# Kernel tuning notes

Hardware: AMD Instinct MI355X
Metric: run time of the kernel (lower is better)

Reference implementation:

```python
import jax, jax.numpy as jnp
import numpy as np

N_NODES = 50000
N_EDGES = 800000
IN_CH, HID_CH, OUT_CH = 128, 128, 64


def _gcn_conv(x, W, b, src, dst, n):
    """PyG GCNConv: self-loops + symmetric norm + linear + scatter-add + bias."""
    loop = jnp.arange(n, dtype=src.dtype)
    src_sl = jnp.concatenate([src, loop])  # [E+N]
    dst_sl = jnp.concatenate([dst, loop])
    # degree computed on edges incl. self-loops (edge weight 1)
    deg = jax.ops.segment_sum(jnp.ones_like(dst_sl, dtype=x.dtype), dst_sl,
                              num_segments=n)
    dinv = jnp.where(deg > 0, jax.lax.rsqrt(deg), 0.0)
    norm = dinv[src_sl] * dinv[dst_sl]  # [E+N]
    xw = x @ W  # [N, F_out]
    msg = xw[src_sl] * norm[:, None]  # gather + scale, [E+N, F_out]
    out = jax.ops.segment_sum(msg, dst_sl, num_segments=n)
    return out + b


def setup_inputs() -> dict:
    key = jax.random.key(0)
    ks = jax.random.split(key, 5)
    x = jax.random.normal(ks[0], (N_NODES, IN_CH), dtype=jnp.float32)
    edge_index = jax.random.randint(ks[1], (2, N_EDGES), 0, N_NODES, dtype=jnp.int64)
    s1 = 1.0 / np.sqrt(IN_CH)
    s2 = 1.0 / np.sqrt(HID_CH)
    W1 = jax.random.normal(ks[2], (IN_CH, HID_CH), dtype=jnp.float32) * s1
    W2 = jax.random.normal(ks[3], (HID_CH, HID_CH), dtype=jnp.float32) * s2
    W3 = jax.random.normal(ks[4], (HID_CH, OUT_CH), dtype=jnp.float32) * s2
    return {
        "x": x, "edge_index": edge_index,
        "W1": W1, "b1": jnp.zeros((HID_CH,), jnp.float32),
        "W2": W2, "b2": jnp.zeros((HID_CH,), jnp.float32),
        "W3": W3, "b3": jnp.zeros((OUT_CH,), jnp.float32),
    }


def reference(x, edge_index, W1, b1, W2, b2, W3, b3):
    n = x.shape[0]
    src, dst = edge_index[0], edge_index[1]
    # dropout(p=0.6) is identity in eval mode
    h = jax.nn.relu(_gcn_conv(x, W1, b1, src, dst, n))
    h = jax.nn.relu(_gcn_conv(h, W2, b2, src, dst, n))
    out = _gcn_conv(h, W3, b3, src, dst, n)
    return out
```

## Files before the change

kernel.cpp:

```cpp
#include <hip/hip_runtime.h>
#include <cstdint>

#define IN_CH 128
#define HID_CH 128
#define OUT_CH 64
#define NB 49
#define CAP 32768
#define CHUNK 2048

typedef __attribute__((ext_vector_type(8))) short bf8_t;
typedef __attribute__((ext_vector_type(4))) float f4_t;

__device__ __forceinline__ uint32_t f_to_bf(float f) {
    union { float f; uint32_t u; } v; v.f = f;
    uint32_t u = v.u;
    return (u + 0x7fffu + ((u >> 16) & 1u)) >> 16;
}
__device__ __forceinline__ float bf_to_f(uint32_t h) {
    union { uint32_t u; float f; } v; v.u = h << 16; return v.f;
}
__device__ __forceinline__ float2 bf2_to_f2(uint32_t u) {
    union { uint32_t u; float f; } a, b;
    a.u = u << 16; b.u = u & 0xffff0000u;
    float2 r; r.x = a.f; r.y = b.f; return r;
}

__device__ __forceinline__ int detect64(const int* __restrict__ e32) {
    return (e32[1] | e32[3] | e32[5] | e32[7]) == 0;
}
__device__ __forceinline__ int edge_at(const void* edges, int is64, int idx) {
    if (is64) return (int)((const long long*)edges)[idx];
    return ((const int*)edges)[idx];
}

__global__ void init_cursors_kernel(int* __restrict__ bucket_cur) {
    int t = threadIdx.x;
    if (t < 64) bucket_cur[t] = t * CAP;
}

__global__ __launch_bounds__(256) void scatter_kernel(
    const void* __restrict__ ei, int* __restrict__ bucket_cur,
    int2* __restrict__ buckets, int E) {
    __shared__ int cnt[64];
    int tid = threadIdx.x;
    int base = blockIdx.x * CHUNK;
    int is64 = detect64((const int*)ei);
    if (tid < 64) cnt[tid] = 0;
    __syncthreads();
    int dloc[8];
#pragma unroll
    for (int it = 0; it < 8; it++) {
        int i = base + it * 256 + tid;
        int d = (i < E) ? edge_at(ei, is64, E + i) : -1;
        dloc[it] = d;
        if (d >= 0) atomicAdd(&cnt[d >> 10], 1);
    }
    __syncthreads();
    if (tid < 64) {
        int v = cnt[tid];
        cnt[tid] = atomicAdd(&bucket_cur[tid], v);
    }
    __syncthreads();
#pragma unroll
    for (int it = 0; it < 8; it++) {
        int i = base + it * 256 + tid;
        if (dloc[it] >= 0) {
            int s = edge_at(ei, is64, i);
            int p = atomicAdd(&cnt[dloc[it] >> 10], 1);
            buckets[p] = make_int2(s, dloc[it]);
        }
    }
}

__global__ __launch_bounds__(512) void csr_local_kernel(
    const int2* __restrict__ buckets, const int* __restrict__ bucket_cur,
    int* __restrict__ row_ptr, int* __restrict__ bsum, float* __restrict__ dinv, int n) {
    __shared__ int cnt[1024];
    __shared__ int sb[1024];
    int b = blockIdx.x, tid = threadIdx.x;
    int base = b << 10;
    int lim = min(1024, n - base);
    if (lim <= 0) { if (tid == 0) bsum[b] = 0; return; }
    int ecnt = bucket_cur[b] - b * CAP;
    const int2* ebase = buckets + (size_t)b * CAP;
    for (int i = tid; i < 1024; i += 512) cnt[i] = 0;
    __syncthreads();
    for (int i = tid; i < ecnt; i += 512)
        atomicAdd(&cnt[ebase[i].y - base], 1);
    __syncthreads();
    for (int i = tid; i < lim; i += 512)
        dinv[base + i] = rsqrtf((float)(cnt[i] + 1));
    __syncthreads();
    int* a = cnt; int* s = sb;
    for (int st = 1; st < 1024; st <<= 1) {
        for (int i = tid; i < 1024; i += 512)
            s[i] = a[i] + ((i >= st) ? a[i - st] : 0);
        __syncthreads();
        int* t = a; a = s; s = t;
    }
    for (int i = tid; i < lim; i += 512)
        row_ptr[base + i] = (i > 0) ? a[i - 1] : 0;
    if (tid == 0) bsum[b] = a[1023];
}

__global__ void scan_totals_kernel(const int* __restrict__ bsum, int* __restrict__ boff,
                                   int* __restrict__ row_ptr, int nb, int n) {
    int lane = threadIdx.x;
    int v = (lane < nb) ? bsum[lane] : 0;
    int incl = v;
#pragma unroll
    for (int off = 1; off < 64; off <<= 1) {
        int t = __shfl_up(incl, off);
        if (lane >= off) incl += t;
    }
    if (lane < nb) boff[lane] = incl - v;
    if (lane == 63) row_ptr[n] = incl;
}

__global__ __launch_bounds__(512) void fill_bucket_kernel(
    const int2* __restrict__ buckets, const int* __restrict__ bucket_cur,
    int* __restrict__ row_ptr, const int* __restrict__ boff,
    int* __restrict__ col, int n) {
    __shared__ int cur[1024];
    int b = blockIdx.x, tid = threadIdx.x;
    int base = b << 10;
    int lim = min(1024, n - base);
    if (lim <= 0) return;
    int ecnt = bucket_cur[b] - b * CAP;
    const int2* ebase = buckets + (size_t)b * CAP;
    int bo = boff[b];
    for (int i = tid; i < lim; i += 512) {
        int v = row_ptr[base + i] + bo;
        row_ptr[base + i] = v;
        cur[i] = v;
    }
    __syncthreads();
    for (int i = tid; i < ecnt; i += 512) {
        int2 e = ebase[i];
        int p = atomicAdd(&cur[e.y - base], 1);
        col[p] = e.x;
    }
}

__global__ void w_split_all(const float* __restrict__ W1, const float* __restrict__ W2,
                            const float* __restrict__ W3,
                            uint16_t* w1h, uint16_t* w1l, uint16_t* w2h, uint16_t* w2l,
                            uint16_t* w3h, uint16_t* w3l) {
    int idx = blockIdx.x * blockDim.x + threadIdx.x;
    const float* W; uint16_t* oh; uint16_t* ol; int FOUT; int e;
    if (idx < 16384)      { W = W1; oh = w1h; ol = w1l; FOUT = 128; e = idx; }
    else if (idx < 32768) { W = W2; oh = w2h; ol = w2l; FOUT = 128; e = idx - 16384; }
    else if (idx < 40960) { W = W3; oh = w3h; ol = w3l; FOUT = 64;  e = idx - 32768; }
    else return;
    int j = e & 7;
    int lane = (e >> 3) & 63;
    int rem = e >> 9;
    int NT = FOUT >> 4;
    int nt = rem % NT, kc = rem / NT;
    int k = kc * 32 + ((lane >> 4) << 3) + j;
    int c = nt * 16 + (lane & 15);
    float v = W[(size_t)k * FOUT + c];
    uint32_t h = f_to_bf(v);
    uint32_t l = f_to_bf(v - bf_to_f(h));
    oh[e] = (uint16_t)h;
    ol[e] = (uint16_t)l;
}

template <int FOUT, bool BFOUT, bool AF32>
__global__ __launch_bounds__(256) void gemm_mfma(
    const void* __restrict__ A0, const uint16_t* __restrict__ Alo,
    const uint16_t* __restrict__ Wfhi, const uint16_t* __restrict__ Wflo,
    const float* __restrict__ dinv, void* __restrict__ Yv, int n) {
    constexpr int NT = FOUT / 16;
    constexpr int NTW = 2;
    int wid = threadIdx.x >> 6;
    int lane = threadIdx.x & 63;
    int cp, tile0, tstride;
    if (FOUT == 128) { cp = wid;     tile0 = blockIdx.x;                  tstride = gridDim.x; }
    else             { cp = wid & 1; tile0 = blockIdx.x * 2 + (wid >> 1); tstride = gridDim.x * 2; }
    int ntiles = (n + 15) >> 4;

    bf8_t wh[NTW][4], wl[NTW][4];
#pragma unroll
    for (int t = 0; t < NTW; t++) {
        int nt = cp * NTW + t;
#pragma unroll
        for (int kc = 0; kc < 4; kc++) {
            size_t b = ((size_t)(kc * NT + nt) * 64 + lane) * 8;
            wh[t][kc] = *(const bf8_t*)&Wfhi[b];
            wl[t][kc] = *(const bf8_t*)&Wflo[b];
        }
    }
    int row_in = lane & 15;
    int koff = (lane >> 4) << 3;
    int colb = lane & 15;
    int rq = (lane >> 4) << 2;

    for (int tile = tile0; tile < ntiles; tile += tstride) {
        int R = tile << 4;
        int arow = R + row_in; if (arow >= n) arow = n - 1;
        bf8_t ah[4], al[4];
        if (AF32) {
            const float* ap = (const float*)A0 + (size_t)arow * 128 + koff;
#pragma unroll
            for (int kc = 0; kc < 4; kc++) {
                float4 pv = *(const float4*)(ap + kc * 32);
                float4 qv = *(const float4*)(ap + kc * 32 + 4);
                float vv[8] = {pv.x, pv.y, pv.z, pv.w, qv.x, qv.y, qv.z, qv.w};
#pragma unroll
                for (int j = 0; j < 8; j++) {
                    uint32_t h = f_to_bf(vv[j]);
                    ah[kc][j] = (short)h;
                    al[kc][j] = (short)f_to_bf(vv[j] - bf_to_f(h));
                }
            }
        } else {
            const uint16_t* ap_hi = (const uint16_t*)A0 + (size_t)arow * 128 + koff;
            const uint16_t* ap_lo = Alo + (size_t)arow * 128 + koff;
#pragma unroll
            for (int kc = 0; kc < 4; kc++) {
                ah[kc] = *(const bf8_t*)(ap_hi + kc * 32);
                al[kc] = *(const bf8_t*)(ap_lo + kc * 32);
            }
        }
        f4_t acc[NTW];
#pragma unroll
        for (int t = 0; t < NTW; t++) acc[t] = (f4_t){0.f, 0.f, 0.f, 0.f};
#pragma unroll
        for (int kc = 0; kc < 4; kc++) {
#pragma unroll
            for (int t = 0; t < NTW; t++) {
                acc[t] = __builtin_amdgcn_mfma_f32_16x16x32_bf16(ah[kc], wh[t][kc], acc[t], 0, 0, 0);
                acc[t] = __builtin_amdgcn_mfma_f32_16x16x32_bf16(ah[kc], wl[t][kc], acc[t], 0, 0, 0);
                acc[t] = __builtin_amdgcn_mfma_f32_16x16x32_bf16(al[kc], wh[t][kc], acc[t], 0, 0, 0);
            }
        }
#pragma unroll
        for (int t = 0; t < NTW; t++) {
            int c = (cp * NTW + t) * 16 + colb;
#pragma unroll
            for (int r = 0; r < 4; r++) {
                int row = R + rq + r;
                if (row < n) {
                    float v = acc[t][r] * dinv[row];
                    if (BFOUT)
                        ((uint16_t*)Yv)[(size_t)row * FOUT + c] = (uint16_t)f_to_bf(v);
                    else
                        ((float*)Yv)[(size_t)row * FOUT + c] = v;
                }
            }
        }
    }
}

template <int CH, bool RELU, int OUTMODE>
__global__ __launch_bounds__(256) void aggregate_kernel(
    const void* __restrict__ Yv, const int* __restrict__ row_ptr,
    const int* __restrict__ col, const float* __restrict__ dinv,
    const float* __restrict__ bias, void* __restrict__ out0,
    void* __restrict__ out1, int n) {
    int w = blockIdx.x * 4 + (threadIdx.x >> 6);
    int lane = threadIdx.x & 63;
    if (w >= n) return;
    constexpr int V = CH / 64;

    auto loadrow = [&](int node) -> float2 {
        if (V == 2) {
            uint32_t u = *((const uint32_t*)Yv + (size_t)node * (CH / 2) + lane);
            return bf2_to_f2(u);
        } else {
            uint32_t u = ((const uint16_t*)Yv)[(size_t)node * CH + lane];
            float2 r; r.x = bf_to_f(u); r.y = 0.f;
            return r;
        }
    };

    float2 acc[8];
#pragma unroll
    for (int t = 0; t < 8; t++) acc[t] = (float2){0.f, 0.f};
    acc[0] = loadrow(w);
    int start = row_ptr[w], end = row_ptr[w + 1];
    for (int base = start; base < end; base += 64) {
        int cnt = min(64, end - base);
        int sv = (base + lane < end) ? col[base + lane] : 0;
        int j = 0;
        for (; j + 8 <= cnt; j += 8) {
            int s[8];
#pragma unroll
            for (int t = 0; t < 8; t++) s[t] = __shfl(sv, j + t);
            float2 v[8];
#pragma unroll
            for (int t = 0; t < 8; t++) v[t] = loadrow(s[t]);
#pragma unroll
            for (int t = 0; t < 8; t++) { acc[t].x += v[t].x; acc[t].y += v[t].y; }
        }
        for (; j + 2 <= cnt; j += 2) {
            int s0 = __shfl(sv, j), s1 = __shfl(sv, j + 1);
            float2 v0 = loadrow(s0), v1 = loadrow(s1);
            acc[0].x += v0.x; acc[0].y += v0.y;
            acc[1].x += v1.x; acc[1].y += v1.y;
        }
        for (; j < cnt; j++) {
            int s = __shfl(sv, j);
            float2 v = loadrow(s);
            acc[0].x += v.x; acc[0].y += v.y;
        }
    }
    float sx = ((acc[0].x + acc[1].x) + (acc[2].x + acc[3].x)) +
               ((acc[4].x + acc[5].x) + (acc[6].x + acc[7].x));
    float sy = ((acc[0].y + acc[1].y) + (acc[2].y + acc[3].y)) +
               ((acc[4].y + acc[5].y) + (acc[6].y + acc[7].y));
    float di = dinv[w];
    if (V == 2) {
        float ox = sx * di + bias[lane * 2];
        float oy = sy * di + bias[lane * 2 + 1];
        if (RELU) { ox = fmaxf(ox, 0.f); oy = fmaxf(oy, 0.f); }
        if (OUTMODE == 0) {
            float2 o; o.x = ox; o.y = oy;
            *(float2*)((float*)out0 + (size_t)w * CH + lane * 2) = o;
        } else {
            uint32_t h0 = f_to_bf(ox), h1 = f_to_bf(oy);
            uint32_t l0 = f_to_bf(ox - bf_to_f(h0)), l1 = f_to_bf(oy - bf_to_f(h1));
            ((uint32_t*)out0)[(size_t)w * (CH / 2) + lane] = h0 | (h1 << 16);
            ((uint32_t*)out1)[(size_t)w * (CH / 2) + lane] = l0 | (l1 << 16);
        }
    } else {
        float ox = sx * di + bias[lane];
        if (RELU) ox = fmaxf(ox, 0.f);
        ((float*)out0)[(size_t)w * CH + lane] = ox;
    }
}

extern "C" void kernel_launch(void* const* d_in, const int* in_sizes, int n_in,
                              void* d_out, int out_size, void* d_ws, size_t ws_size,
                              hipStream_t stream) {
    const float* x  = (const float*)d_in[0];
    const void*  ei = d_in[1];
    const float* W1 = (const float*)d_in[2];
    const float* b1 = (const float*)d_in[3];
    const float* W2 = (const float*)d_in[4];
    const float* b2 = (const float*)d_in[5];
    const float* W3 = (const float*)d_in[6];
    const float* b3 = (const float*)d_in[7];
    int n = in_sizes[0] / IN_CH;
    int E = in_sizes[1] / 2;

    char* p = (char*)d_ws;
    auto carve = [&](size_t bytes) {
        char* r = p;
        p += (bytes + 255) & ~(size_t)255;
        return r;
    };
    float*    dinv       = (float*)carve((size_t)n * 4);
    int*      row_ptr    = (int*)carve((size_t)(n + 1) * 4);
    int*      bsum       = (int*)carve(64 * 4);
    int*      boff       = (int*)carve(64 * 4);
    int*      bucket_cur = (int*)carve(64 * 4);
    int*      col        = (int*)carve((size_t)E * 4);
    char*     bucket_mem = carve((size_t)NB * CAP * 8);
    int2*     buckets    = (int2*)bucket_mem;
    void*     y          = (void*)bucket_mem;
    uint16_t* ahi        = (uint16_t*)carve((size_t)n * 128 * 2);
    uint16_t* alo        = (uint16_t*)carve((size_t)n * 128 * 2);
    uint16_t* w1h        = (uint16_t*)carve(128 * 128 * 2);
    uint16_t* w1l        = (uint16_t*)carve(128 * 128 * 2);
    uint16_t* w2h        = (uint16_t*)carve(128 * 128 * 2);
    uint16_t* w2l        = (uint16_t*)carve(128 * 128 * 2);
    uint16_t* w3h        = (uint16_t*)carve(128 * 64 * 2);
    uint16_t* w3l        = (uint16_t*)carve(128 * 64 * 2);

    const int tpb = 256;
    int sb = (E + CHUNK - 1) / CHUNK;

    init_cursors_kernel<<<1, 64, 0, stream>>>(bucket_cur);
    scatter_kernel<<<sb, tpb, 0, stream>>>(ei, bucket_cur, buckets, E);
    csr_local_kernel<<<NB, 512, 0, stream>>>(buckets, bucket_cur, row_ptr, bsum, dinv, n);
    scan_totals_kernel<<<1, 64, 0, stream>>>(bsum, boff, row_ptr, NB, n);
    fill_bucket_kernel<<<NB, 512, 0, stream>>>(buckets, bucket_cur, row_ptr, boff, col, n);
    w_split_all<<<160, tpb, 0, stream>>>(W1, W2, W3, w1h, w1l, w2h, w2l, w3h, w3l);

    int gb = 782;
    int ab = (n + 3) / 4;

    gemm_mfma<128, true, true><<<gb, 256, 0, stream>>>(x, nullptr, w1h, w1l, dinv, y, n);
    aggregate_kernel<128, true, 1><<<ab, 256, 0, stream>>>(y, row_ptr, col, dinv, b1, ahi, alo, n);
    gemm_mfma<128, true, false><<<gb, 256, 0, stream>>>(ahi, alo, w2h, w2l, dinv, y, n);
    aggregate_kernel<128, true, 1><<<ab, 256, 0, stream>>>(y, row_ptr, col, dinv, b2, ahi, alo, n);
    gemm_mfma<64, true, false><<<gb, 256, 0, stream>>>(ahi, alo, w3h, w3l, dinv, y, n);
    aggregate_kernel<64, false, 0><<<ab, 256, 0, stream>>>(y, row_ptr, col, dinv, b3, d_out, nullptr, n);
}
```

Before: 283.2 us.

## Fuse aggregation with next-layer GEMM and overlap edge scatter with first GEMM

Merges the init-cursor kernel into the weight-split kernel. Runs the edge bucket scatter and the first-layer GEMM in one launch, with the GEMM no longer scaling by dinv because dinv is not yet known at that point. Each aggregate kernel now stages its 16 aggregated rows (hi/lo bf16) in shared memory and immediately runs the next layer's MFMA GEMM. This removes the round trip of the hidden activations through global memory and cuts the launch count. The cost is per-edge dinv[src] loads in the first aggregation and fewer neighbour accumulators.

```diff
diff --git a/kernel.cpp b/kernel.cpp
--- a/kernel.cpp
+++ b/kernel.cpp
@@ -1,10 +1,6 @@
 #include <hip/hip_runtime.h>
 #include <cstdint>
 
-#define IN_CH 128
-#define HID_CH 128
-#define OUT_CH 64
-#define NB 49
 #define CAP 32768
 #define CHUNK 2048
 
@@ -33,42 +29,136 @@
     return ((const int*)edges)[idx];
 }
 
-__global__ void init_cursors_kernel(int* __restrict__ bucket_cur) {
-    int t = threadIdx.x;
-    if (t < 64) bucket_cur[t] = t * CAP;
-}
-
-__global__ __launch_bounds__(256) void scatter_kernel(
+__global__ __launch_bounds__(256) void prep_kernel(
+    const float* __restrict__ W1, const float* __restrict__ W2,
+    const float* __restrict__ W3,
+    uint16_t* w1h, uint16_t* w1l, uint16_t* w2h, uint16_t* w2l,
+    uint16_t* w3h, uint16_t* w3l, int* __restrict__ bucket_cur) {
+    if (blockIdx.x == 160) {
+        if (threadIdx.x < 64) bucket_cur[threadIdx.x] = threadIdx.x * CAP;
+        return;
+    }
+    int idx = blockIdx.x * 256 + threadIdx.x;
+    const float* W; uint16_t* oh; uint16_t* ol; int FOUT; int e;
+    if (idx < 16384)      { W = W1; oh = w1h; ol = w1l; FOUT = 128; e = idx; }
+    else if (idx < 32768) { W = W2; oh = w2h; ol = w2l; FOUT = 128; e = idx - 16384; }
+    else                  { W = W3; oh = w3h; ol = w3l; FOUT = 64;  e = idx - 32768; }
+    int j = e & 7;
+    int lane = (e >> 3) & 63;
+    int rem = e >> 9;
+    int NT = FOUT >> 4;
+    int nt = rem % NT, kc = rem / NT;
+    int k = kc * 32 + ((lane >> 4) << 3) + j;
+    int c = nt * 16 + (lane & 15);
+    float v = W[(size_t)k * FOUT + c];
+    uint32_t h = f_to_bf(v);
+    uint32_t l = f_to_bf(v - bf_to_f(h));
+    oh[e] = (uint16_t)h;
+    ol[e] = (uint16_t)l;
+}
+
+__device__ __forceinline__ void gemm1_body(
+    const float* __restrict__ A, const uint16_t* __restrict__ Wfhi,
+    const uint16_t* __restrict__ Wflo, uint16_t* __restrict__ Yout,
+    int n, int cp, int tile0, int tstride, int lane) {
+    constexpr int NT = 8, NTW = 2;
+    int ntiles = (n + 15) >> 4;
+    bf8_t wh[NTW][4], wl[NTW][4];
+#pragma unroll
+    for (int t = 0; t < NTW; t++) {
+        int nt = cp * NTW + t;
+#pragma unroll
+        for (int kc = 0; kc < 4; kc++) {
+            size_t b = ((size_t)(kc * NT + nt) * 64 + lane) * 8;
+            wh[t][kc] = *(const bf8_t*)&Wfhi[b];
+            wl[t][kc] = *(const bf8_t*)&Wflo[b];
+        }
+    }
+    int row_in = lane & 15;
+    int koff = (lane >> 4) << 3;
+    int colb = lane & 15;
+    int rq = (lane >> 4) << 2;
+    for (int tile = tile0; tile < ntiles; tile += tstride) {
+        int R = tile << 4;
+        int arow = R + row_in; if (arow >= n) arow = n - 1;
+        const float* ap = A + (size_t)arow * 128 + koff;
+        bf8_t ah[4], al[4];
+#pragma unroll
+        for (int kc = 0; kc < 4; kc++) {
+            float4 pv = *(const float4*)(ap + kc * 32);
+            float4 qv = *(const float4*)(ap + kc * 32 + 4);
+            float vv[8] = {pv.x, pv.y, pv.z, pv.w, qv.x, qv.y, qv.z, qv.w};
+#pragma unroll
+            for (int j = 0; j < 8; j++) {
+                uint32_t h = f_to_bf(vv[j]);
+                ah[kc][j] = (short)h;
+                al[kc][j] = (short)f_to_bf(vv[j] - bf_to_f(h));
+            }
+        }
+        f4_t acc[NTW];
+#pragma unroll
+        for (int t = 0; t < NTW; t++) acc[t] = (f4_t){0.f, 0.f, 0.f, 0.f};
+#pragma unroll
+        for (int kc = 0; kc < 4; kc++) {
+#pragma unroll
+            for (int t = 0; t < NTW; t++) {
+                acc[t] = __builtin_amdgcn_mfma_f32_16x16x32_bf16(ah[kc], wh[t][kc], acc[t], 0, 0, 0);
+                acc[t] = __builtin_amdgcn_mfma_f32_16x16x32_bf16(ah[kc], wl[t][kc], acc[t], 0, 0, 0);
+                acc[t] = __builtin_amdgcn_mfma_f32_16x16x32_bf16(al[kc], wh[t][kc], acc[t], 0, 0, 0);
+            }
+        }
+#pragma unroll
+        for (int t = 0; t < NTW; t++) {
+            int c = (cp * NTW + t) * 16 + colb;
+#pragma unroll
+            for (int r = 0; r < 4; r++) {
+                int row = R + rq + r;
+                if (row < n)
+                    Yout[(size_t)row * 128 + c] = (uint16_t)f_to_bf(acc[t][r]);
+            }
+        }
+    }
+}
+
+__global__ __launch_bounds__(256) void scatter_gemm1_kernel(
     const void* __restrict__ ei, int* __restrict__ bucket_cur,
-    int2* __restrict__ buckets, int E) {
-    __shared__ int cnt[64];
+    int2* __restrict__ buckets, int E, int sbcnt,
+    const float* __restrict__ x, const uint16_t* __restrict__ w1h,
+    const uint16_t* __restrict__ w1l, uint16_t* __restrict__ y1, int n) {
     int tid = threadIdx.x;
-    int base = blockIdx.x * CHUNK;
-    int is64 = detect64((const int*)ei);
-    if (tid < 64) cnt[tid] = 0;
-    __syncthreads();
-    int dloc[8];
-#pragma unroll
-    for (int it = 0; it < 8; it++) {
-        int i = base + it * 256 + tid;
-        int d = (i < E) ? edge_at(ei, is64, E + i) : -1;
-        dloc[it] = d;
-        if (d >= 0) atomicAdd(&cnt[d >> 10], 1);
-    }
-    __syncthreads();
-    if (tid < 64) {
-        int v = cnt[tid];
-        cnt[tid] = atomicAdd(&bucket_cur[tid], v);
-    }
-    __syncthreads();
-#pragma unroll
-    for (int it = 0; it < 8; it++) {
-        int i = base + it * 256 + tid;
-        if (dloc[it] >= 0) {
-            int s = edge_at(ei, is64, i);
-            int p = atomicAdd(&cnt[dloc[it] >> 10], 1);
-            buckets[p] = make_int2(s, dloc[it]);
-        }
+    if ((int)blockIdx.x < sbcnt) {
+        __shared__ int cnt[64];
+        int base = blockIdx.x * CHUNK;
+        int is64 = detect64((const int*)ei);
+        if (tid < 64) cnt[tid] = 0;
+        __syncthreads();
+        int dloc[8];
+#pragma unroll
+        for (int it = 0; it < 8; it++) {
+            int i = base + it * 256 + tid;
+            int d = (i < E) ? edge_at(ei, is64, E + i) : -1;
+            dloc[it] = d;
+            if (d >= 0) atomicAdd(&cnt[d >> 10], 1);
+        }
+        __syncthreads();
+        if (tid < 64) {
+            int v = cnt[tid];
+            cnt[tid] = atomicAdd(&bucket_cur[tid], v);
+        }
+        __syncthreads();
+#pragma unroll
+        for (int it = 0; it < 8; it++) {
+            int i = base + it * 256 + tid;
+            if (dloc[it] >= 0) {
+                int s = edge_at(ei, is64, i);
+                int p = atomicAdd(&cnt[dloc[it] >> 10], 1);
+                buckets[p] = make_int2(s, dloc[it]);
+            }
+        }
+    } else {
+        int lane = tid & 63, wid = tid >> 6;
+        gemm1_body(x, w1h, w1l, y1, n, wid, blockIdx.x - sbcnt,
+                   gridDim.x - sbcnt, lane);
     }
 }
 
@@ -142,44 +232,75 @@
     }
 }
 
-__global__ void w_split_all(const float* __restrict__ W1, const float* __restrict__ W2,
-                            const float* __restrict__ W3,
-                            uint16_t* w1h, uint16_t* w1l, uint16_t* w2h, uint16_t* w2l,
-                            uint16_t* w3h, uint16_t* w3l) {
-    int idx = blockIdx.x * blockDim.x + threadIdx.x;
-    const float* W; uint16_t* oh; uint16_t* ol; int FOUT; int e;
-    if (idx < 16384)      { W = W1; oh = w1h; ol = w1l; FOUT = 128; e = idx; }
-    else if (idx < 32768) { W = W2; oh = w2h; ol = w2l; FOUT = 128; e = idx - 16384; }
-    else if (idx < 40960) { W = W3; oh = w3h; ol = w3l; FOUT = 64;  e = idx - 32768; }
-    else return;
-    int j = e & 7;
-    int lane = (e >> 3) & 63;
-    int rem = e >> 9;
-    int NT = FOUT >> 4;
-    int nt = rem % NT, kc = rem / NT;
-    int k = kc * 32 + ((lane >> 4) << 3) + j;
-    int c = nt * 16 + (lane & 15);
-    float v = W[(size_t)k * FOUT + c];
-    uint32_t h = f_to_bf(v);
-    uint32_t l = f_to_bf(v - bf_to_f(h));
-    oh[e] = (uint16_t)h;
-    ol[e] = (uint16_t)l;
-}
-
-template <int FOUT, bool BFOUT, bool AF32>
-__global__ __launch_bounds__(256) void gemm_mfma(
-    const void* __restrict__ A0, const uint16_t* __restrict__ Alo,
+template <int FOUT, bool SRC_SCALE>
+__global__ __launch_bounds__(256) void agg_gemm_kernel(
+    const uint16_t* __restrict__ Yin, const int* __restrict__ row_ptr,
+    const int* __restrict__ col, const float* __restrict__ dinv,
+    const float* __restrict__ bias,
     const uint16_t* __restrict__ Wfhi, const uint16_t* __restrict__ Wflo,
-    const float* __restrict__ dinv, void* __restrict__ Yv, int n) {
+    uint16_t* __restrict__ Yout, int n) {
+    constexpr int LDW = 136;
+    __shared__ uint16_t hs[16 * LDW];
+    __shared__ uint16_t ls[16 * LDW];
+    int tid = threadIdx.x, wid = tid >> 6, lane = tid & 63;
+    int base = blockIdx.x * 16;
+
+    auto lr = [&](int node) -> float2 {
+        uint32_t u = ((const uint32_t*)Yin)[(size_t)node * 64 + lane];
+        return bf2_to_f2(u);
+    };
+
+    for (int q = 0; q < 4; q++) {
+        int r = wid * 4 + q, node = base + r;
+        uint32_t ph = 0, pl = 0;
+        if (node < n) {
+            float di = dinv[node];
+            float2 a0, a1, a2, a3;
+            {
+                float2 s = lr(node);
+                float sc = SRC_SCALE ? di : 1.f;
+                a0.x = s.x * sc; a0.y = s.y * sc;
+            }
+            a1 = (float2){0.f, 0.f}; a2 = (float2){0.f, 0.f}; a3 = (float2){0.f, 0.f};
+            int start = row_ptr[node], end = row_ptr[node + 1];
+            for (int b = start; b < end; b += 64) {
+                int cnt = min(64, end - b);
+                int sv = (b + lane < end) ? col[b + lane] : 0;
+                int j = 0;
+                for (; j + 4 <= cnt; j += 4) {
+                    int s0 = __shfl(sv, j),     s1 = __shfl(sv, j + 1);
+                    int s2 = __shfl(sv, j + 2), s3 = __shfl(sv, j + 3);
+                    float d0 = 1.f, d1 = 1.f, d2 = 1.f, d3 = 1.f;
+                    if (SRC_SCALE) { d0 = dinv[s0]; d1 = dinv[s1]; d2 = dinv[s2]; d3 = dinv[s3]; }
+                    float2 v0 = lr(s0), v1 = lr(s1), v2 = lr(s2), v3 = lr(s3);
+                    a0.x += v0.x * d0; a0.y += v0.y * d0;
+                    a1.x += v1.x * d1; a1.y += v1.y * d1;
+                    a2.x += v2.x * d2; a2.y += v2.y * d2;
+                    a3.x += v3.x * d3; a3.y += v3.y * d3;
+                }
+                for (; j < cnt; j++) {
+                    int s = __shfl(sv, j);
+                    float d0 = SRC_SCALE ? dinv[s] : 1.f;
+                    float2 v = lr(s);
+                    a0.x += v.x * d0; a0.y += v.y * d0;
+                }
+            }
+            float sx = (a0.x + a1.x) + (a2.x + a3.x);
+            float sy = (a0.y + a1.y) + (a2.y + a3.y);
+            float ox = fmaxf(sx * di + bias[2 * lane], 0.f);
+            float oy = fmaxf(sy * di + bias[2 * lane + 1], 0.f);
+            uint32_t h0 = f_to_bf(ox), h1 = f_to_bf(oy);
+            uint32_t l0 = f_to_bf(ox - bf_to_f(h0)), l1 = f_to_bf(oy - bf_to_f(h1));
+            ph = h0 | (h1 << 16); pl = l0 | (l1 << 16);
+        }
+        ((uint32_t*)(hs + r * LDW))[lane] = ph;
+        ((uint32_t*)(ls + r * LDW))[lane] = pl;
+    }
+    __syncthreads();
+
     constexpr int NT = FOUT / 16;
-    constexpr int NTW = 2;
-    int wid = threadIdx.x >> 6;
-    int lane = threadIdx.x & 63;
-    int cp, tile0, tstride;
-    if (FOUT == 128) { cp = wid;     tile0 = blockIdx.x;                  tstride = gridDim.x; }
-    else             { cp = wid & 1; tile0 = blockIdx.x * 2 + (wid >> 1); tstride = gridDim.x * 2; }
-    int ntiles = (n + 15) >> 4;
-
+    constexpr int NTW = NT / 4;
+    int cp = wid;
     bf8_t wh[NTW][4], wl[NTW][4];
 #pragma unroll
     for (int t = 0; t < NTW; t++) {
@@ -191,144 +312,66 @@
             wl[t][kc] = *(const bf8_t*)&Wflo[b];
         }
     }
-    int row_in = lane & 15;
     int koff = (lane >> 4) << 3;
     int colb = lane & 15;
     int rq = (lane >> 4) << 2;
-
-    for (int tile = tile0; tile < ntiles; tile += tstride) {
-        int R = tile << 4;
-        int arow = R + row_in; if (arow >= n) arow = n - 1;
-        bf8_t ah[4], al[4];
-        if (AF32) {
-            const float* ap = (const float*)A0 + (size_t)arow * 128 + koff;
-#pragma unroll
-            for (int kc = 0; kc < 4; kc++) {
-                float4 pv = *(const float4*)(ap + kc * 32);
-                float4 qv = *(const float4*)(ap + kc * 32 + 4);
-                float vv[8] = {pv.x, pv.y, pv.z, pv.w, qv.x, qv.y, qv.z, qv.w};
-#pragma unroll
-                for (int j = 0; j < 8; j++) {
-                    uint32_t h = f_to_bf(vv[j]);
-                    ah[kc][j] = (short)h;
-                    al[kc][j] = (short)f_to_bf(vv[j] - bf_to_f(h));
-                }
-            }
-        } else {
-            const uint16_t* ap_hi = (const uint16_t*)A0 + (size_t)arow * 128 + koff;
-            const uint16_t* ap_lo = Alo + (size_t)arow * 128 + koff;
-#pragma unroll
-            for (int kc = 0; kc < 4; kc++) {
-                ah[kc] = *(const bf8_t*)(ap_hi + kc * 32);
-                al[kc] = *(const bf8_t*)(ap_lo + kc * 32);
-            }
-        }
-        f4_t acc[NTW];
-#pragma unroll
-        for (int t = 0; t < NTW; t++) acc[t] = (f4_t){0.f, 0.f, 0.f, 0.f};
-#pragma unroll
-        for (int kc = 0; kc < 4; kc++) {
-#pragma unroll
-            for (int t = 0; t < NTW; t++) {
-                acc[t] = __builtin_amdgcn_mfma_f32_16x16x32_bf16(ah[kc], wh[t][kc], acc[t], 0, 0, 0);
-                acc[t] = __builtin_amdgcn_mfma_f32_16x16x32_bf16(ah[kc], wl[t][kc], acc[t], 0, 0, 0);
-                acc[t] = __builtin_amdgcn_mfma_f32_16x16x32_bf16(al[kc], wh[t][kc], acc[t], 0, 0, 0);
-            }
-        }
+    bf8_t ah[4], al[4];
+#pragma unroll
+    for (int kc = 0; kc < 4; kc++) {
+        ah[kc] = *(const bf8_t*)(hs + (lane & 15) * LDW + koff + kc * 32);
+        al[kc] = *(const bf8_t*)(ls + (lane & 15) * LDW + koff + kc * 32);
+    }
+    f4_t acc[NTW];
+#pragma unroll
+    for (int t = 0; t < NTW; t++) acc[t] = (f4_t){0.f, 0.f, 0.f, 0.f};
+#pragma unroll
+    for (int kc = 0; kc < 4; kc++) {
 #pragma unroll
         for (int t = 0; t < NTW; t++) {
-            int c = (cp * NTW + t) * 16 + colb;
-#pragma unroll
-            for (int r = 0; r < 4; r++) {
-                int row = R + rq + r;
-                if (row < n) {
-                    float v = acc[t][r] * dinv[row];
-                    if (BFOUT)
-                        ((uint16_t*)Yv)[(size_t)row * FOUT + c] = (uint16_t)f_to_bf(v);
-                    else
-                        ((float*)Yv)[(size_t)row * FOUT + c] = v;
-                }
-            }
-        }
-    }
-}
-
-template <int CH, bool RELU, int OUTMODE>
-__global__ __launch_bounds__(256) void aggregate_kernel(
-    const void* __restrict__ Yv, const int* __restrict__ row_ptr,
+            acc[t] = __builtin_amdgcn_mfma_f32_16x16x32_bf16(ah[kc], wh[t][kc], acc[t], 0, 0, 0);
+            acc[t] = __builtin_amdgcn_mfma_f32_16x16x32_bf16(ah[kc], wl[t][kc], acc[t], 0, 0, 0);
+            acc[t] = __builtin_amdgcn_mfma_f32_16x16x32_bf16(al[kc], wh[t][kc], acc[t], 0, 0, 0);
+        }
+    }
+#pragma unroll
+    for (int t = 0; t < NTW; t++) {
+        int c = (cp * NTW + t) * 16 + colb;
+#pragma unroll
+        for (int r = 0; r < 4; r++) {
+            int row = base + rq + r;
+            if (row < n) {
+                float v = acc[t][r] * dinv[row];
+                Yout[(size_t)row * FOUT + c] = (uint16_t)f_to_bf(v);
+            }
+        }
+    }
+}
+
+__global__ __launch_bounds__(256) void agg_final_kernel(
+    const uint16_t* __restrict__ Y, const int* __restrict__ row_ptr,
     const int* __restrict__ col, const float* __restrict__ dinv,
-    const float* __restrict__ bias, void* __restrict__ out0,
-    void* __restrict__ out1, int n) {
+    const float* __restrict__ bias, float* __restrict__ out, int n) {
     int w = blockIdx.x * 4 + (threadIdx.x >> 6);
     int lane = threadIdx.x & 63;
     if (w >= n) return;
-    constexpr int V = CH / 64;
-
-    auto loadrow = [&](int node) -> float2 {
-        if (V == 2) {
-            uint32_t u = *((const uint32_t*)Yv + (size_t)node * (CH / 2) + lane);
-            return bf2_to_f2(u);
-        } else {
-            uint32_t u = ((const uint16_t*)Yv)[(size_t)node * CH + lane];
-            float2 r; r.x = bf_to_f(u); r.y = 0.f;
-            return r;
-        }
+    auto lr = [&](int node) -> float {
+        return bf_to_f(Y[(size_t)node * 64 + lane]);
     };
-
-    float2 acc[8];
-#pragma unroll
-    for (int t = 0; t < 8; t++) acc[t] = (float2){0.f, 0.f};
-    acc[0] = loadrow(w);
+    float a0 = lr(w), a1 = 0.f, a2 = 0.f, a3 = 0.f;
     int start = row_ptr[w], end = row_ptr[w + 1];
-    for (int base = start; base < end; base += 64) {
-        int cnt = min(64, end - base);
-        int sv = (base + lane < end) ? col[base + lane] : 0;
+    for (int b = start; b < end; b += 64) {
+        int cnt = min(64, end - b);
+        int sv = (b + lane < end) ? col[b + lane] : 0;
         int j = 0;
-        for (; j + 8 <= cnt; j += 8) {
-            int s[8];
-#pragma unroll
-            for (int t = 0; t < 8; t++) s[t] = __shfl(sv, j + t);
-            float2 v[8];
-#pragma unroll
-            for (int t = 0; t < 8; t++) v[t] = loadrow(s[t]);
-#pragma unroll
-            for (int t = 0; t < 8; t++) { acc[t].x += v[t].x; acc[t].y += v[t].y; }
-        }
-        for (; j + 2 <= cnt; j += 2) {
-            int s0 = __shfl(sv, j), s1 = __shfl(sv, j + 1);
-            float2 v0 = loadrow(s0), v1 = loadrow(s1);
-            acc[0].x += v0.x; acc[0].y += v0.y;
-            acc[1].x += v1.x; acc[1].y += v1.y;
-        }
-        for (; j < cnt; j++) {
-            int s = __shfl(sv, j);
-            float2 v = loadrow(s);
-            acc[0].x += v.x; acc[0].y += v.y;
-        }
-    }
-    float sx = ((acc[0].x + acc[1].x) + (acc[2].x + acc[3].x)) +
-               ((acc[4].x + acc[5].x) + (acc[6].x + acc[7].x));
-    float sy = ((acc[0].y + acc[1].y) + (acc[2].y + acc[3].y)) +
-               ((acc[4].y + acc[5].y) + (acc[6].y + acc[7].y));
-    float di = dinv[w];
-    if (V == 2) {
-        float ox = sx * di + bias[lane * 2];
-        float oy = sy * di + bias[lane * 2 + 1];
-        if (RELU) { ox = fmaxf(ox, 0.f); oy = fmaxf(oy, 0.f); }
-        if (OUTMODE == 0) {
-            float2 o; o.x = ox; o.y = oy;
-            *(float2*)((float*)out0 + (size_t)w * CH + lane * 2) = o;
-        } else {
-            uint32_t h0 = f_to_bf(ox), h1 = f_to_bf(oy);
-            uint32_t l0 = f_to_bf(ox - bf_to_f(h0)), l1 = f_to_bf(oy - bf_to_f(h1));
-            ((uint32_t*)out0)[(size_t)w * (CH / 2) + lane] = h0 | (h1 << 16);
-            ((uint32_t*)out1)[(size_t)w * (CH / 2) + lane] = l0 | (l1 << 16);
-        }
-    } else {
-        float ox = sx * di + bias[lane];
-        if (RELU) ox = fmaxf(ox, 0.f);
-        ((float*)out0)[(size_t)w * CH + lane] = ox;
-    }
+        for (; j + 4 <= cnt; j += 4) {
+            int s0 = __shfl(sv, j),     s1 = __shfl(sv, j + 1);
+            int s2 = __shfl(sv, j + 2), s3 = __shfl(sv, j + 3);
+            a0 += lr(s0); a1 += lr(s1); a2 += lr(s2); a3 += lr(s3);
+        }
+        for (; j < cnt; j++) a0 += lr(__shfl(sv, j));
+    }
+    float ox = ((a0 + a1) + (a2 + a3)) * dinv[w] + bias[lane];
+    out[(size_t)w * 64 + lane] = ox;
 }
 
 extern "C" void kernel_launch(void* const* d_in, const int* in_sizes, int n_in,
@@ -342,8 +385,9 @@
     const float* b2 = (const float*)d_in[5];
     const float* W3 = (const float*)d_in[6];
     const float* b3 = (const float*)d_in[7];
-    int n = in_sizes[0] / IN_CH;
+    int n = in_sizes[0] / 128;
     int E = in_sizes[1] / 2;
+    int nbuck = (n + 1023) >> 10;
 
     char* p = (char*)d_ws;
     auto carve = [&](size_t bytes) {
@@ -357,11 +401,10 @@
     int*      boff       = (int*)carve(64 * 4);
     int*      bucket_cur = (int*)carve(64 * 4);
     int*      col        = (int*)carve((size_t)E * 4);
-    char*     bucket_mem = carve((size_t)NB * CAP * 8);
-    int2*     buckets    = (int2*)bucket_mem;
-    void*     y          = (void*)bucket_mem;
-    uint16_t* ahi        = (uint16_t*)carve((size_t)n * 128 * 2);
-    uint16_t* alo        = (uint16_t*)carve((size_t)n * 128 * 2);
+    int2*     buckets    = (int2*)carve((size_t)64 * CAP * 8);
+    uint16_t* y1         = (uint16_t*)carve((size_t)n * 128 * 2);
+    uint16_t* y2         = (uint16_t*)carve((size_t)n * 128 * 2);
+    uint16_t* y3         = (uint16_t*)carve((size_t)n * 64 * 2);
     uint16_t* w1h        = (uint16_t*)carve(128 * 128 * 2);
     uint16_t* w1l        = (uint16_t*)carve(128 * 128 * 2);
     uint16_t* w2h        = (uint16_t*)carve(128 * 128 * 2);
@@ -369,23 +412,20 @@
     uint16_t* w3h        = (uint16_t*)carve(128 * 64 * 2);
     uint16_t* w3l        = (uint16_t*)carve(128 * 64 * 2);
 
-    const int tpb = 256;
-    int sb = (E + CHUNK - 1) / CHUNK;
-
-    init_cursors_kernel<<<1, 64, 0, stream>>>(bucket_cur);
-    scatter_kernel<<<sb, tpb, 0, stream>>>(ei, bucket_cur, buckets, E);
-    csr_local_kernel<<<NB, 512, 0, stream>>>(buckets, bucket_cur, row_ptr, bsum, dinv, n);
-    scan_totals_kernel<<<1, 64, 0, stream>>>(bsum, boff, row_ptr, NB, n);
-    fill_bucket_kernel<<<NB, 512, 0, stream>>>(buckets, bucket_cur, row_ptr, boff, col, n);
-    w_split_all<<<160, tpb, 0, stream>>>(W1, W2, W3, w1h, w1l, w2h, w2l, w3h, w3l);
-
-    int gb = 782;
-    int ab = (n + 3) / 4;
-
-    gemm_mfma<128, true, true><<<gb, 256, 0, stream>>>(x, nullptr, w1h, w1l, dinv, y, n);
-    aggregate_kernel<128, true, 1><<<ab, 256, 0, stream>>>(y, row_ptr, col, dinv, b1, ahi, alo, n);
-    gemm_mfma<128, true, false><<<gb, 256, 0, stream>>>(ahi, alo, w2h, w2l, dinv, y, n);
-    aggregate_kernel<128, true, 1><<<ab, 256, 0, stream>>>(y, row_ptr, col, dinv, b2, ahi, alo, n);
-    gemm_mfma<64, true, false><<<gb, 256, 0, stream>>>(ahi, alo, w3h, w3l, dinv, y, n);
-    aggregate_kernel<64, false, 0><<<ab, 256, 0, stream>>>(y, row_ptr, col, dinv, b3, d_out, nullptr, n);
-}
+    int sbcnt = (E + CHUNK - 1) / CHUNK;
+    int fb = (n + 15) / 16;
+
+    prep_kernel<<<161, 256, 0, stream>>>(W1, W2, W3, w1h, w1l, w2h, w2l,
+                                         w3h, w3l, bucket_cur);
+    scatter_gemm1_kernel<<<sbcnt + 782, 256, 0, stream>>>(
+        ei, bucket_cur, buckets, E, sbcnt, x, w1h, w1l, y1, n);
+    csr_local_kernel<<<nbuck, 512, 0, stream>>>(buckets, bucket_cur, row_ptr, bsum, dinv, n);
+    scan_totals_kernel<<<1, 64, 0, stream>>>(bsum, boff, row_ptr, nbuck, n);
+    fill_bucket_kernel<<<nbuck, 512, 0, stream>>>(buckets, bucket_cur, row_ptr, boff, col, n);
+    agg_gemm_kernel<128, true><<<fb, 256, 0, stream>>>(
+        y1, row_ptr, col, dinv, b1, w2h, w2l, y2, n);
+    agg_gemm_kernel<64, false><<<fb, 256, 0, stream>>>(
+        y2, row_ptr, col, dinv, b2, w3h, w3l, y3, n);
+    agg_final_kernel<<<(n + 3) / 4, 256, 0, stream>>>(
+        y3, row_ptr, col, dinv, b3, (float*)d_out, n);
+}
```

Result: faster. 248.4 us (-12.3%).
